# Performance work log

Measured on AMD Instinct MI355X. Metric: run time of the kernel, lower is better.

The kernel has to match this reference:

```python
import jax, jax.numpy as jnp
import numpy as np

KH, KW = 3, 3          # kernel_size
STRIDE, PAD, DIL = 1, 1, 1
DG = 1                 # deformable_groups


def setup_inputs() -> dict:
    key = jax.random.key(0)
    k1, k2 = jax.random.split(key)
    x = jax.random.normal(k1, (4, 64, 128, 128), dtype=jnp.float32)
    # offset layout: [B, 2*DG*KH*KW, Ho, Wo], pairs are (dy, dx) per tap
    offset = jax.random.normal(k2, (4, 2 * DG * KH * KW, 128, 128), dtype=jnp.float32)
    return {"input": x, "offset": offset}


def _deform_unfold(x, offset):
    B, C, H, W = x.shape
    Ho = (H + 2 * PAD - DIL * (KH - 1) - 1) // STRIDE + 1
    Wo = (W + 2 * PAD - DIL * (KW - 1) - 1) // STRIDE + 1
    K = KH * KW
    Cg = C // DG

    off = offset.reshape(B, DG, K, 2, Ho, Wo)
    oy, ox = off[:, :, :, 0], off[:, :, :, 1]          # [B,DG,K,Ho,Wo]

    # tap displacements within the kernel window
    ky = (jnp.repeat(jnp.arange(KH), KW) * DIL).astype(x.dtype)  # [K]
    kx = (jnp.tile(jnp.arange(KW), KH) * DIL).astype(x.dtype)    # [K]
    gy = (jnp.arange(Ho) * STRIDE - PAD).astype(x.dtype)         # [Ho]
    gx = (jnp.arange(Wo) * STRIDE - PAD).astype(x.dtype)         # [Wo]

    # fractional sampling coordinates  [B,DG,K,Ho,Wo]
    py = oy + gy[None, None, None, :, None] + ky[None, None, :, None, None]
    px = ox + gx[None, None, None, None, :] + kx[None, None, :, None, None]

    y0 = jnp.floor(py)
    x0 = jnp.floor(px)
    wy1 = py - y0
    wx1 = px - x0
    wy0 = 1.0 - wy1
    wx0 = 1.0 - wx1
    y0i = y0.astype(jnp.int32)
    x0i = x0.astype(jnp.int32)

    x_flat = x.reshape(B, DG, Cg, H * W)

    def corner(yi, xi, w):
        valid = ((yi >= 0) & (yi < H) & (xi >= 0) & (xi < W)).astype(x.dtype)
        idx = jnp.clip(yi, 0, H - 1) * W + jnp.clip(xi, 0, W - 1)   # [B,DG,K,Ho,Wo]
        idxf = idx.reshape(B, DG, K * Ho * Wo)
        # gather: xf [Cg,HW], ix [N] -> [Cg,N]; vmapped over B and DG
        g = jax.vmap(jax.vmap(lambda xf, ix: xf[:, ix]))(x_flat, idxf)
        g = g.reshape(B, DG, Cg, K, Ho, Wo)
        return g * (w * valid)[:, :, None]        # broadcast over Cg

    out = (corner(y0i, x0i, wy0 * wx0)
           + corner(y0i, x0i + 1, wy0 * wx1)
           + corner(y0i + 1, x0i, wy1 * wx0)
           + corner(y0i + 1, x0i + 1, wy1 * wx1))   # [B,DG,Cg,K,Ho,Wo]

    # im2col layout: channel-major, tap-minor -> [B, C*K, Ho*Wo]
    return out.reshape(B, C * K, Ho * Wo)


def reference(input, offset):
    return _deform_unfold(input, offset)
```

## Files before the change

### kernel.cpp

```cpp
#include <hip/hip_runtime.h>


#define BB 4
#define CC 64
#define HH 128
#define WW 128
#define KK 9
#define HW (HH * WW)
#define NR 16
#define CG 8
#define NG (CC / CG)
#define TPB 256

__global__ __launch_bounds__(TPB) void deform_unfold_lds(
    const float* __restrict__ x, const float* __restrict__ off,
    float* __restrict__ out)
{
    __shared__ float2 tile[NR * WW];
    __shared__ int anyfall;

    int tid = threadIdx.x;
    int bid = blockIdx.x;
    int g = bid & (NG - 1);
    int t = (bid >> 3) & 63;
    int b = bid >> 9;

    int s  = t * TPB + tid;
    int wo = s & (WW - 1);
    int ho = s >> 7;
    int r0 = 2 * t - 6;
    r0 = min(max(r0, 0), HH - NR);

    if (tid == 0) anyfall = 0;
    __syncthreads();

    float u0[KK], u1[KK], t0w[KK], t1w[KK];
    int aA[KK], aB[KK];
    int myfall = 0;
    #pragma unroll
    for (int k = 0; k < KK; ++k) {
        int ky = k / 3, kx = k - ky * 3;
        float oy = off[(((size_t)b * (2 * KK)) + 2 * k) * HW + s];
        float ox = off[(((size_t)b * (2 * KK)) + 2 * k + 1) * HW + s];
        float py = oy + (float)(ho - 1 + ky);
        float px = ox + (float)(wo - 1 + kx);
        float y0f = floorf(py), x0f = floorf(px);
        float wy1 = py - y0f, wx1 = px - x0f;
        float wy0 = 1.f - wy1, wx0 = 1.f - wx1;
        int y0 = (int)y0f, x0 = (int)x0f;
        int y1 = y0 + 1, x1 = x0 + 1;
        bool vy0 = (y0 >= 0) && (y0 < HH), vy1 = (y1 >= 0) && (y1 < HH);
        bool vx0 = (x0 >= 0) && (x0 < WW), vx1 = (x1 >= 0) && (x1 < WW);
        int y0c = min(max(y0, 0), HH - 1), y1c = min(max(y1, 0), HH - 1);
        int xa  = min(max(x0, 0), WW - 2);
        int i0  = min(max(x0, 0), WW - 1) - xa;
        int i1  = min(max(x1, 0), WW - 1) - xa;
        float w00 = wy0 * wx0 * ((vy0 && vx0) ? 1.f : 0.f);
        float w01 = wy0 * wx1 * ((vy0 && vx1) ? 1.f : 0.f);
        float w10 = wy1 * wx0 * ((vy1 && vx0) ? 1.f : 0.f);
        float w11 = wy1 * wx1 * ((vy1 && vx1) ? 1.f : 0.f);
        u0[k]  = (i0 == 0 ? w00 : 0.f) + (i1 == 0 ? w01 : 0.f);
        u1[k]  = (i0 == 1 ? w00 : 0.f) + (i1 == 1 ? w01 : 0.f);
        t0w[k] = (i0 == 0 ? w10 : 0.f) + (i1 == 0 ? w11 : 0.f);
        t1w[k] = (i0 == 1 ? w10 : 0.f) + (i1 == 1 ? w11 : 0.f);
        int rA = y0c - r0, rB = y1c - r0;
        myfall |= ((unsigned)rA >= NR) | ((unsigned)rB >= NR);
        rA = min(max(rA, 0), NR - 1);
        rB = min(max(rB, 0), NR - 1);
        aA[k] = rA * WW + xa;
        aB[k] = rB * WW + xa;
    }
    if (myfall) atomicOr(&anyfall, 1);
    __syncthreads();
    bool fall = (anyfall != 0);

    int c0g = g * CG;
    const float* xb = x + ((size_t)b * CC + c0g) * HW;
    float* ob = out + (((size_t)b * CC + c0g) * KK) * HW + s;

    if (!fall) {
        for (int cp = 0; cp < CG / 2; ++cp) {
            const float4* s0 = (const float4*)(xb + ((size_t)(2 * cp)) * HW + (size_t)r0 * WW);
            const float4* s1 = (const float4*)(xb + ((size_t)(2 * cp) + 1) * HW + (size_t)r0 * WW);
            float4 a0 = s0[2 * tid], a1 = s0[2 * tid + 1];
            float4 b0 = s1[2 * tid], b1 = s1[2 * tid + 1];
            __syncthreads();
            float2* w = &tile[8 * tid];
            w[0] = make_float2(a0.x, b0.x); w[1] = make_float2(a0.y, b0.y);
            w[2] = make_float2(a0.z, b0.z); w[3] = make_float2(a0.w, b0.w);
            w[4] = make_float2(a1.x, b1.x); w[5] = make_float2(a1.y, b1.y);
            w[6] = make_float2(a1.z, b1.z); w[7] = make_float2(a1.w, b1.w);
            __syncthreads();
            float* o = ob + (size_t)(2 * cp) * KK * HW;
            #pragma unroll
            for (int k = 0; k < KK; ++k) {
                float2 p00 = tile[aA[k]], p01 = tile[aA[k] + 1];
                float2 p10 = tile[aB[k]], p11 = tile[aB[k] + 1];
                float vx_ = p00.x * u0[k] + p01.x * u1[k] + p10.x * t0w[k] + p11.x * t1w[k];
                float vy_ = p00.y * u0[k] + p01.y * u1[k] + p10.y * t0w[k] + p11.y * t1w[k];
                o[(size_t)k * HW] = vx_;
                o[(size_t)(KK * HW) + (size_t)k * HW] = vy_;
            }
        }
    } else {
        #pragma unroll 1
        for (int k = 0; k < KK; ++k) {
            int ky = k / 3, kx = k - ky * 3;
            float oy = off[(((size_t)b * (2 * KK)) + 2 * k) * HW + s];
            float ox = off[(((size_t)b * (2 * KK)) + 2 * k + 1) * HW + s];
            float py = oy + (float)(ho - 1 + ky);
            float px = ox + (float)(wo - 1 + kx);
            float y0f = floorf(py), x0f = floorf(px);
            float wy1 = py - y0f, wx1 = px - x0f;
            float wy0 = 1.f - wy1, wx0 = 1.f - wx1;
            int y0 = (int)y0f, x0 = (int)x0f;
            int y1 = y0 + 1, x1 = x0 + 1;
            bool vy0 = (y0 >= 0) && (y0 < HH), vy1 = (y1 >= 0) && (y1 < HH);
            bool vx0 = (x0 >= 0) && (x0 < WW), vx1 = (x1 >= 0) && (x1 < WW);
            int y0c = min(max(y0, 0), HH - 1), y1c = min(max(y1, 0), HH - 1);
            int x0c = min(max(x0, 0), WW - 1), x1c = min(max(x1, 0), WW - 1);
            float w00 = wy0 * wx0 * ((vy0 && vx0) ? 1.f : 0.f);
            float w01 = wy0 * wx1 * ((vy0 && vx1) ? 1.f : 0.f);
            float w10 = wy1 * wx0 * ((vy1 && vx0) ? 1.f : 0.f);
            float w11 = wy1 * wx1 * ((vy1 && vx1) ? 1.f : 0.f);
            int o00 = y0c * WW + x0c, o01 = y0c * WW + x1c;
            int o10 = y1c * WW + x0c, o11 = y1c * WW + x1c;
            #pragma unroll 1
            for (int c = 0; c < CG; ++c) {
                const float* xc = xb + (size_t)c * HW;
                (ob + (size_t)c * KK * HW)[(size_t)k * HW] =
                    xc[o00] * w00 + xc[o01] * w01 + xc[o10] * w10 + xc[o11] * w11;
            }
        }
    }
}

extern "C" void kernel_launch(void* const* d_in, const int* in_sizes, int n_in,
                              void* d_out, int out_size, void* d_ws, size_t ws_size,
                              hipStream_t stream) {
    const float* x   = (const float*)d_in[0];
    const float* off = (const float*)d_in[1];
    float* out = (float*)d_out;

    int blocks = BB * 64 * NG;
    deform_unfold_lds<<<blocks, TPB, 0, stream>>>(x, off, out);
}
```

Baseline: 39.88 us.

## Prefetch next channel pair into registers and use nontemporal output stores

New measurement: 37.97 us (median of 2 runs). 4.8% less time.

```diff
diff --git a/kernel.cpp b/kernel.cpp
--- a/kernel.cpp
+++ b/kernel.cpp
@@ -12,30 +12,41 @@
 #define NG (CC / CG)
 #define TPB 256
 
-__global__ __launch_bounds__(TPB) void deform_unfold_lds(
+__global__ __launch_bounds__(TPB, 4) void deform_unfold_lds(
     const float* __restrict__ x, const float* __restrict__ off,
     float* __restrict__ out)
 {
     __shared__ float2 tile[NR * WW];
     __shared__ int anyfall;
 
-    int tid = threadIdx.x;
-    int bid = blockIdx.x;
-    int g = bid & (NG - 1);
-    int t = (bid >> 3) & 63;
-    int b = bid >> 9;
+    const int tid = threadIdx.x;
+    const int bid = blockIdx.x;
+    const int g = bid & (NG - 1);
+    const int t = (bid >> 3) & 63;
+    const int b = bid >> 9;
 
-    int s  = t * TPB + tid;
-    int wo = s & (WW - 1);
-    int ho = s >> 7;
-    int r0 = 2 * t - 6;
-    r0 = min(max(r0, 0), HH - NR);
+    const int s  = t * TPB + tid;
+    const int wo = s & (WW - 1);
+    const int ho = s >> 7;
+    const int r0 = min(max(2 * t - 6, 0), HH - NR);
+
+    const int c0g = g * CG;
+    const float* xb = x + ((size_t)b * CC + c0g) * HW;
+    float* ob = out + (((size_t)b * CC + c0g) * KK) * HW + s;
+
+    float2 pa[4], pb[4];
+    {
+        const float2* A2 = (const float2*)(xb + (size_t)r0 * WW);
+        const float2* B2 = (const float2*)(xb + HW + (size_t)r0 * WW);
+        #pragma unroll
+        for (int j = 0; j < 4; ++j) { pa[j] = A2[tid + 256 * j]; pb[j] = B2[tid + 256 * j]; }
+    }
 
     if (tid == 0) anyfall = 0;
     __syncthreads();
 
     float u0[KK], u1[KK], t0w[KK], t1w[KK];
-    int aA[KK], aB[KK];
+    int aAB[KK];
     int myfall = 0;
     #pragma unroll
     for (int k = 0; k < KK; ++k) {
@@ -67,40 +78,38 @@
         myfall |= ((unsigned)rA >= NR) | ((unsigned)rB >= NR);
         rA = min(max(rA, 0), NR - 1);
         rB = min(max(rB, 0), NR - 1);
-        aA[k] = rA * WW + xa;
-        aB[k] = rB * WW + xa;
+        aAB[k] = (rA * WW + xa) | ((rB * WW + xa) << 16);
     }
     if (myfall) atomicOr(&anyfall, 1);
     __syncthreads();
-    bool fall = (anyfall != 0);
-
-    int c0g = g * CG;
-    const float* xb = x + ((size_t)b * CC + c0g) * HW;
-    float* ob = out + (((size_t)b * CC + c0g) * KK) * HW + s;
+    const bool fall = (anyfall != 0);
 
     if (!fall) {
+        #pragma unroll
         for (int cp = 0; cp < CG / 2; ++cp) {
-            const float4* s0 = (const float4*)(xb + ((size_t)(2 * cp)) * HW + (size_t)r0 * WW);
-            const float4* s1 = (const float4*)(xb + ((size_t)(2 * cp) + 1) * HW + (size_t)r0 * WW);
-            float4 a0 = s0[2 * tid], a1 = s0[2 * tid + 1];
-            float4 b0 = s1[2 * tid], b1 = s1[2 * tid + 1];
-            __syncthreads();
-            float2* w = &tile[8 * tid];
-            w[0] = make_float2(a0.x, b0.x); w[1] = make_float2(a0.y, b0.y);
-            w[2] = make_float2(a0.z, b0.z); w[3] = make_float2(a0.w, b0.w);
-            w[4] = make_float2(a1.x, b1.x); w[5] = make_float2(a1.y, b1.y);
-            w[6] = make_float2(a1.z, b1.z); w[7] = make_float2(a1.w, b1.w);
+            float4* wt = (float4*)tile;
+            #pragma unroll
+            for (int j = 0; j < 4; ++j)
+                wt[tid + 256 * j] = make_float4(pa[j].x, pb[j].x, pa[j].y, pb[j].y);
+            if (cp + 1 < CG / 2) {
+                const float2* A2 = (const float2*)(xb + (size_t)(2 * cp + 2) * HW + (size_t)r0 * WW);
+                const float2* B2 = (const float2*)(xb + (size_t)(2 * cp + 3) * HW + (size_t)r0 * WW);
+                #pragma unroll
+                for (int j = 0; j < 4; ++j) { pa[j] = A2[tid + 256 * j]; pb[j] = B2[tid + 256 * j]; }
+            }
             __syncthreads();
             float* o = ob + (size_t)(2 * cp) * KK * HW;
             #pragma unroll
             for (int k = 0; k < KK; ++k) {
-                float2 p00 = tile[aA[k]], p01 = tile[aA[k] + 1];
-                float2 p10 = tile[aB[k]], p11 = tile[aB[k] + 1];
+                int aA = aAB[k] & 0xffff, aB = aAB[k] >> 16;
+                float2 p00 = tile[aA], p01 = tile[aA + 1];
+                float2 p10 = tile[aB], p11 = tile[aB + 1];
                 float vx_ = p00.x * u0[k] + p01.x * u1[k] + p10.x * t0w[k] + p11.x * t1w[k];
                 float vy_ = p00.y * u0[k] + p01.y * u1[k] + p10.y * t0w[k] + p11.y * t1w[k];
-                o[(size_t)k * HW] = vx_;
-                o[(size_t)(KK * HW) + (size_t)k * HW] = vy_;
+                __builtin_nontemporal_store(vx_, o + (size_t)k * HW);
+                __builtin_nontemporal_store(vy_, o + (size_t)(KK + k) * HW);
             }
+            __syncthreads();
         }
     } else {
         #pragma unroll 1
```
